# Optimization experiments

Hardware: AMD Instinct MI355X
Metric: run time of the kernel (lower is better)

The kernel has to match this reference:

```python
import jax, jax.numpy as jnp
import numpy as np

DIM = 1024
NH = 8
HD = DIM // NH  # 128
E = 8
EPS = 1e-5


def rope_cos_sin(L, hd):
    # matches RotaryPositionEmbedding: emb = cat([freqs, freqs], -1)
    inv_freq = 1.0 / (10000.0 ** (jnp.arange(0, hd, 2, dtype=jnp.float32) / hd))
    freqs = jnp.arange(L, dtype=jnp.float32)[:, None] * inv_freq[None, :]  # (L, hd/2)
    emb = jnp.concatenate([freqs, freqs], axis=-1)  # (L, hd)
    return jnp.cos(emb), jnp.sin(emb)


def rotate_half(x):
    # interleaved rotate, as in the torch apply_rope
    x1 = x[..., 0::2]
    x2 = x[..., 1::2]
    return jnp.stack((-x2, x1), axis=-1).reshape(x.shape)


def rope(t, cos, sin):
    # t: (B,H,L,D); cos/sin: (L,D)
    return t * cos[None, None] + rotate_half(t) * sin[None, None]


def heads(t):
    B, L, C = t.shape
    return t.reshape(B, L, NH, HD).transpose(0, 2, 1, 3)  # (B,H,L,D)


def setup_inputs() -> dict:
    key = jax.random.key(0)
    ks = jax.random.split(key, 32)
    std = 0.02
    d = {}
    d['x'] = jax.random.normal(ks[0], (16, 512, DIM), jnp.float32)
    d['h_a'] = jax.random.normal(ks[1], (16, 256, DIM), jnp.float32)
    d['h_t'] = jax.random.normal(ks[2], (16, 256, DIM), jnp.float32)
    names = ['qa', 'ka', 'va', 'qt', 'kt', 'vt', 'o', 'ffn']
    for i, n in enumerate(names):
        d['W_' + n] = jax.random.normal(ks[3 + 2 * i], (E, DIM, DIM), jnp.float32) * std
        d['b_' + n] = jax.random.normal(ks[4 + 2 * i], (E, DIM), jnp.float32) * std
    d['gamma'] = jnp.ones((E, DIM), jnp.float32)
    d['beta'] = jnp.zeros((E, DIM), jnp.float32)
    d['gating_factor'] = jnp.zeros((E,), jnp.float32)
    d['expert_idx'] = 3
    return d


def reference(x, h_a, h_t,
              W_qa, b_qa, W_ka, b_ka, W_va, b_va,
              W_qt, b_qt, W_kt, b_kt, W_vt, b_vt,
              W_o, b_o, W_ffn, b_ffn,
              gamma, beta, gating_factor, expert_idx):
    e = expert_idx

    def lin(t, W, b):
        return t @ W[e].T + b[e]

    B, T, C = x.shape
    Ka = h_a.shape[1]
    Kt = h_t.shape[1]

    q_a = heads(lin(x, W_qa, b_qa))        # (B,H,T,D)
    q_t = heads(lin(x, W_qt, b_qt))
    k_a = heads(lin(h_a, W_ka, b_ka))      # (B,H,Ka,D)
    v_a = heads(lin(h_a, W_va, b_va))
    k_t = heads(lin(h_t, W_kt, b_kt))      # (B,H,Kt,D)
    v_t = heads(lin(h_t, W_vt, b_vt))

    cos_m, sin_m = rope_cos_sin(T, HD)
    q_a = rope(q_a, cos_m, sin_m)
    q_t = rope(q_t, cos_m, sin_m)
    cos_a, sin_a = rope_cos_sin(Ka, HD)
    k_a = rope(k_a, cos_a, sin_a)
    cos_t, sin_t = rope_cos_sin(Kt, HD)
    k_t = rope(k_t, cos_t, sin_t)

    ratio_g = jax.nn.sigmoid(gating_factor[e])
    s_a = jnp.einsum('bhtd,bhkd->bhtk', q_a, k_a)
    s_t = jnp.einsum('bhtd,bhkd->bhtk', q_t, k_t) * ratio_g
    scores = jnp.concatenate([s_a, s_t], axis=-1) / np.sqrt(HD)
    w = jax.nn.softmax(scores, axis=-1)            # (B,H,T,Ka+Kt)
    v = jnp.concatenate([v_a, v_t], axis=2)        # (B,H,Ka+Kt,D)
    out = jnp.einsum('bhtk,bhkd->bhtd', w, v)
    out = out.transpose(0, 2, 1, 3).reshape(B, T, C)
    out = lin(out, W_o, b_o)

    x = out + x
    # ffn: SmileMoENorm -> SmileMoELinear -> ReLU (no extra residual)
    mu = jnp.mean(x, axis=-1, keepdims=True)
    var = jnp.var(x, axis=-1, keepdims=True)
    xn = (x - mu) / jnp.sqrt(var + EPS) * gamma[e] + beta[e]
    x = jax.nn.relu(lin(xn, W_ffn, b_ffn))
    return x
```

## Files before the change

kernel.cpp:

```cpp
#include <hip/hip_runtime.h>
#include <stdint.h>

typedef __bf16 bf16x8 __attribute__((ext_vector_type(8)));
typedef float f32x4 __attribute__((ext_vector_type(4)));
typedef unsigned short u16x8 __attribute__((ext_vector_type(8)));

typedef const __attribute__((address_space(1))) void* gas_ptr;
typedef __attribute__((address_space(3))) void* las_ptr;
typedef const __attribute__((address_space(3))) char* lds_c3;

__device__ __forceinline__ void gload16(const void* g, void* l) {
  __builtin_amdgcn_global_load_lds((gas_ptr)g, (las_ptr)l, 16, 0, 0);
}

__device__ __forceinline__ bf16x8 dsread16(const char* p) {
  bf16x8 r;
  asm volatile("ds_read_b128 %0, %1" : "=v"(r) : "v"((lds_c3)p));
  return r;
}
__device__ __forceinline__ void dswrite2(char* p, uint32_t v) {
  asm volatile("ds_write_b16 %0, %1" : : "v"((las_ptr)p), "v"(v));
}
template <int OFF>
__device__ __forceinline__ float dswz(float x) {
  float r;
  asm volatile("ds_swizzle_b32 %0, %1 offset:%c2" : "=v"(r) : "v"(x), "i"(OFF));
  return r;
}

__device__ __forceinline__ unsigned short f2bf(float f) {
  uint32_t u = __float_as_uint(f);
  u += 0x7FFFu + ((u >> 16) & 1u);
  return (unsigned short)(u >> 16);
}

__device__ __forceinline__ void conv8(const float* __restrict__ src,
                                      unsigned short* __restrict__ dst, int i) {
  const float4* s4 = (const float4*)src;
  float4 a = s4[2 * i], b = s4[2 * i + 1];
  u16x8 r;
  r[0] = f2bf(a.x); r[1] = f2bf(a.y); r[2] = f2bf(a.z); r[3] = f2bf(a.w);
  r[4] = f2bf(b.x); r[5] = f2bf(b.y); r[6] = f2bf(b.z); r[7] = f2bf(b.w);
  *(u16x8*)&dst[(size_t)i * 8] = r;
}

__global__ __launch_bounds__(256)
void prep_all(const float* __restrict__ x, const float* __restrict__ h_a,
              const float* __restrict__ h_t,
              const float* W0, const float* W1, const float* W2, const float* W3,
              const float* W4, const float* W5, const float* W6, const float* W7,
              const int* __restrict__ eptr,
              unsigned short* __restrict__ XB, unsigned short* __restrict__ HAB,
              unsigned short* __restrict__ HTB, unsigned short* __restrict__ WW,
              float* __restrict__ cosb, float* __restrict__ sinb) {
  const int blk = blockIdx.x, tid = threadIdx.x;
  if (blk < 4096) {
    conv8(x, XB, blk * 256 + tid);
  } else if (blk < 6144) {
    conv8(h_a, HAB, (blk - 4096) * 256 + tid);
  } else if (blk < 8192) {
    conv8(h_t, HTB, (blk - 6144) * 256 + tid);
  } else if (blk < 12288) {
    const int w = (blk - 8192) >> 9;
    const int i = ((blk - 8192) & 511) * 256 + tid;
    const float* wp;
    switch (w) {
      case 0: wp = W0; break; case 1: wp = W1; break;
      case 2: wp = W2; break; case 3: wp = W3; break;
      case 4: wp = W4; break; case 5: wp = W5; break;
      case 6: wp = W6; break; default: wp = W7; break;
    }
    conv8(wp + (size_t)(*eptr) * 1048576, WW + (size_t)w * 1048576, i);
  } else {
    const int i = (blk - 12288) * 256 + tid;
    const int t = i >> 7, d = i & 127;
    const int f = d & 63;
    float invf = expf(-0.14391156831212787f * (float)f);
    float ang = (float)t * invf;
    float s, c;
    sincosf(ang, &s, &c);
    cosb[i] = c;
    sinb[i] = s;
  }
}

template <int MODE>
__global__ __launch_bounds__(512, 1)
void gemm8p(const unsigned short* __restrict__ A0, const unsigned short* __restrict__ A1,
            const unsigned short* __restrict__ W0, const unsigned short* __restrict__ W1,
            const unsigned short* __restrict__ W2, const unsigned short* __restrict__ W3,
            const float* __restrict__ bias0, const float* __restrict__ bias1,
            const float* __restrict__ bias2, const float* __restrict__ bias3,
            const int* __restrict__ eptr, const float* __restrict__ ctab,
            const float* __restrict__ stab,
            unsigned short* __restrict__ out0, unsigned short* __restrict__ out1,
            unsigned short* __restrict__ outV) {
  __shared__ __align__(16) char AL[65536];
  __shared__ __align__(16) char BL[65536];
  const int tid = threadIdx.x;
  const int lane = tid & 63, wid = tid >> 6, fr = lane & 15, g = lane >> 4;
  const int wm = wid >> 2, wn = wid & 3;
  const int id = blockIdx.x;
  constexpr int CPX = (MODE == 0) ? 32 : 16;
  const int swz = (id & 7) * CPX + (id >> 3);
  const int bm = swz >> 3, bn = swz & 7;
  const int z = (MODE == 1) ? blockIdx.y : 0;
  const int e = *eptr;

  const unsigned short* Asel;
  const unsigned short* Wsel;
  const float* bias;
  const int half = bn >> 2;
  const int cb0 = (bn & 3) * 256;
  if constexpr (MODE == 0) {
    Asel = A0;
    Wsel = half ? W1 : W0;
    bias = (half ? bias1 : bias0) + e * 1024;
  } else {
    Asel = z ? A1 : A0;
    Wsel = z ? (half ? W3 : W2) : (half ? W1 : W0);
    bias = (z ? (half ? bias3 : bias2) : (half ? bias1 : bias0)) + e * 1024;
  }

  const char* Ab = (const char*)Asel + (size_t)bm * 256 * 2048;
  const char* Bb = (const char*)Wsel + (size_t)cb0 * 2048;

  const int csw = (((tid & 7) ^ (((tid >> 3) & 1) << 2) ^ (((tid >> 5) & 1) << 1)) << 4);
  const char* Ags = Ab + (tid >> 3) * 2048 + csw;
  const char* Bgs = Bb + (tid >> 3) * 2048 + csw;
  char* Ald = AL + tid * 16;
  char* Bld = BL + tid * 16;

#define STA(T)                                                              \
  { const char* s_ = Ags + (T) * 128;                                       \
    char* d_ = Ald + ((T) & 1) * 32768;                                     \
    gload16(s_, d_);           gload16(s_ + 131072, d_ + 8192);             \
    gload16(s_ + 262144, d_ + 16384); gload16(s_ + 393216, d_ + 24576); }
#define STB(T)                                                              \
  { const char* s_ = Bgs + (T) * 128;                                       \
    char* d_ = Bld + ((T) & 1) * 32768;                                     \
    gload16(s_, d_);           gload16(s_ + 131072, d_ + 8192);             \
    gload16(s_ + 262144, d_ + 16384); gload16(s_ + 393216, d_ + 24576); }

  const int lsw = ((fr & 1) << 2) ^ (((fr >> 2) & 1) << 1);
  const int cs0 = ((0 * 4 + g) ^ lsw) << 4;
  const int cs1 = ((1 * 4 + g) ^ lsw) << 4;
  const int arow = (wm * 128 + fr) * 128;
  const int brow = (wn * 64 + fr) * 128;

  f32x4 acc[8][4];
#pragma unroll
  for (int m = 0; m < 8; ++m)
#pragma unroll
    for (int n = 0; n < 4; ++n) acc[m][n] = f32x4{0.f, 0.f, 0.f, 0.f};
  bf16x8 af[8], bfr[2];

#define RDA(BUF, CS)                                                        \
  { const char* p_ = AL + (BUF) * 32768 + arow + (CS);                      \
    _Pragma("unroll") for (int m = 0; m < 8; ++m)                           \
        af[m] = dsread16(p_ + m * 2048); }
#define RDB(BUF, CS, NH)                                                    \
  { const char* p_ = BL + (BUF) * 32768 + brow + (NH) * 4096 + (CS);        \
    bfr[0] = dsread16(p_);                                                  \
    bfr[1] = dsread16(p_ + 2048); }

#define MF16(NH)                                                            \
  __builtin_amdgcn_s_setprio(1);                                            \
  _Pragma("unroll") for (int m = 0; m < 8; ++m) {                           \
    acc[m][(NH)*2]   = __builtin_amdgcn_mfma_f32_16x16x32_bf16(             \
        af[m], bfr[0], acc[m][(NH)*2], 0, 0, 0);                            \
    acc[m][(NH)*2+1] = __builtin_amdgcn_mfma_f32_16x16x32_bf16(             \
        af[m], bfr[1], acc[m][(NH)*2+1], 0, 0, 0);                          \
  }                                                                         \
  __builtin_amdgcn_s_setprio(0);

#define SB __builtin_amdgcn_sched_barrier(0)
#define BAR __builtin_amdgcn_s_barrier()
#define LGK0 asm volatile("s_waitcnt lgkmcnt(0)")

  STA(0); STB(0);
  SB;
  asm volatile("s_waitcnt vmcnt(0)");
  BAR;

#pragma unroll 1
  for (int t = 0; t < 16; ++t) {
    const int buf = t & 1;
    RDA(buf, cs0); RDB(buf, cs0, 0); SB;
    if (t < 15) STA(t + 1);
    SB; BAR; LGK0; SB;
    MF16(0) SB; BAR;
    RDB(buf, cs0, 1); SB;
    if (t < 15) STB(t + 1);
    SB; BAR; LGK0; SB;
    MF16(1) SB; BAR;
    RDA(buf, cs1); RDB(buf, cs1, 0); SB;
    BAR; LGK0; SB;
    MF16(0) SB; BAR;
    RDB(buf, cs1, 1); SB;
    BAR; LGK0; SB;
    MF16(1) SB;
    if (t < 15) { asm volatile("s_waitcnt vmcnt(0)"); }
    BAR;
  }
#undef RDA
#undef RDB
#undef MF16
#undef STA
#undef STB

  const int wrow0 = bm * 256 + wm * 128;
#pragma unroll
  for (int m = 0; m < 8; ++m) {
#pragma unroll
    for (int n = 0; n < 4; ++n) {
      const int gc = cb0 + wn * 64 + n * 16 + fr;
      const float bv = bias[gc];
#pragma unroll
      for (int j = 0; j < 4; ++j) {
        const int grow = wrow0 + m * 16 + g * 4 + j;
        float v = acc[m][n][j] + bv;
        if constexpr (MODE == 0) {
          const int t = grow & 511, bb = grow >> 9;
          const int hh = gc >> 7, dd = gc & 127;
          float pv = __shfl_xor(v, 1);
          float cs = ctab[t * 128 + dd], sn = stab[t * 128 + dd];
          float rh = (dd & 1) ? pv : -pv;
          float o = v * cs + rh * sn;
          unsigned short* dst = half ? out1 : out0;
          dst[(((size_t)(bb * 8 + hh) * 512 + t) << 7) + dd] = f2bf(o);
        } else {
          const int t = grow & 255, bb = grow >> 8;
          const int hh = gc >> 7, dd = gc & 127;
          if (half == 0) {
            float pv = __shfl_xor(v, 1);
            float cs = ctab[t * 128 + dd], sn = stab[t * 128 + dd];
            float rh = (dd & 1) ? pv : -pv;
            float o = v * cs + rh * sn;
            unsigned short* dst = z ? out1 : out0;
            dst[(((size_t)(bb * 8 + hh) * 256 + t) << 7) + dd] = f2bf(o);
          } else {
            outV[(((size_t)(bb * 8 + hh) << 7) + dd) * 512 + z * 256 + t] = f2bf(v);
          }
        }
      }
    }
  }
}

template <int MODE>
__global__ __launch_bounds__(512, 1)
void gemm4p(const unsigned short* __restrict__ A, const unsigned short* __restrict__ W,
            const float* __restrict__ biasb, const int* __restrict__ eptr,
            const float* __restrict__ resid, float* __restrict__ outf) {
  __shared__ __align__(16) char AL[65536];
  __shared__ __align__(16) char BL[32768];
  const int tid = threadIdx.x;
  const int lane = tid & 63, wid = tid >> 6, fr = lane & 15, g = lane >> 4;
  const int wm = wid >> 1, wn = wid & 1;
  const int id = blockIdx.x;
  const int swz = (id & 7) * 32 + (id >> 3);
  const int bm = swz >> 3, bn = swz & 7;
  const int e = *eptr;
  const float* bias = biasb + e * 1024;

  const char* Ab = (const char*)A + (size_t)bm * 256 * 2048;
  const char* Bb = (const char*)W + (size_t)bn * 128 * 2048;

  const int csw = (((tid & 7) ^ (((tid >> 3) & 1) << 2) ^ (((tid >> 5) & 1) << 1)) << 4);
  const char* Ags = Ab + (tid >> 3) * 2048 + csw;
  const char* Bgs = Bb + (tid >> 3) * 2048 + csw;
  char* Ald = AL + tid * 16;
  char* Bld = BL + tid * 16;

#define STA4(T)                                                             \
  { const char* s_ = Ags + (T) * 128;                                       \
    char* d_ = Ald + ((T) & 1) * 32768;                                     \
    gload16(s_, d_);           gload16(s_ + 131072, d_ + 8192);             \
    gload16(s_ + 262144, d_ + 16384); gload16(s_ + 393216, d_ + 24576); }
#define STB4(T)                                                             \
  { const char* s_ = Bgs + (T) * 128;                                       \
    char* d_ = Bld + ((T) & 1) * 16384;                                     \
    gload16(s_, d_);           gload16(s_ + 131072, d_ + 8192); }

  const int lsw = ((fr & 1) << 2) ^ (((fr >> 2) & 1) << 1);
  const int cs0 = ((0 * 4 + g) ^ lsw) << 4;
  const int cs1 = ((1 * 4 + g) ^ lsw) << 4;
  const int arow = (wm * 64 + fr) * 128;
  const int brow = (wn * 64 + fr) * 128;

  f32x4 acc[4][4];
#pragma unroll
  for (int m = 0; m < 4; ++m)
#pragma unroll
    for (int n = 0; n < 4; ++n) acc[m][n] = f32x4{0.f, 0.f, 0.f, 0.f};
  bf16x8 af[4], bfr[2];

#define RDA4(BUF, CS)                                                       \
  { const char* p_ = AL + (BUF) * 32768 + arow + (CS);                      \
    _Pragma("unroll") for (int m = 0; m < 4; ++m)                           \
        af[m] = dsread16(p_ + m * 2048); }
#define RDB4(BUF, CS, NH)                                                   \
  { const char* p_ = BL + (BUF) * 16384 + brow + (NH) * 4096 + (CS);        \
    bfr[0] = dsread16(p_);                                                  \
    bfr[1] = dsread16(p_ + 2048); }

#define MF8(NH)                                                             \
  __builtin_amdgcn_s_setprio(1);                                            \
  _Pragma("unroll") for (int m = 0; m < 4; ++m) {                           \
    acc[m][(NH)*2]   = __builtin_amdgcn_mfma_f32_16x16x32_bf16(             \
        af[m], bfr[0], acc[m][(NH)*2], 0, 0, 0);                            \
    acc[m][(NH)*2+1] = __builtin_amdgcn_mfma_f32_16x16x32_bf16(             \
        af[m], bfr[1], acc[m][(NH)*2+1], 0, 0, 0);                          \
  }                                                                         \
  __builtin_amdgcn_s_setprio(0);

  STA4(0); STB4(0);
  __builtin_amdgcn_sched_barrier(0);
  asm volatile("s_waitcnt vmcnt(0)");
  __builtin_amdgcn_s_barrier();

#pragma unroll 1
  for (int t = 0; t < 16; ++t) {
    const int buf = t & 1;
    RDA4(buf, cs0); RDB4(buf, cs0, 0); SB;
    if (t < 15) STA4(t + 1);
    SB; BAR; LGK0; SB;
    MF8(0) SB; BAR;
    RDB4(buf, cs0, 1); SB;
    if (t < 15) STB4(t + 1);
    SB; BAR; LGK0; SB;
    MF8(1) SB; BAR;
    RDA4(buf, cs1); RDB4(buf, cs1, 0); SB;
    BAR; LGK0; SB;
    MF8(0) SB; BAR;
    RDB4(buf, cs1, 1); SB;
    BAR; LGK0; SB;
    MF8(1) SB;
    if (t < 15) { asm volatile("s_waitcnt vmcnt(0)"); }
    BAR;
  }
#undef RDA4
#undef RDB4
#undef MF8
#undef STA4
#undef STB4
#undef SB
#undef BAR
#undef LGK0

  const int wrow0 = bm * 256 + wm * 64;
#pragma unroll
  for (int m = 0; m < 4; ++m) {
#pragma unroll
    for (int n = 0; n < 4; ++n) {
      const int gc = bn * 128 + wn * 64 + n * 16 + fr;
      const float bv = bias[gc];
#pragma unroll
      for (int j = 0; j < 4; ++j) {
        const int grow = wrow0 + m * 16 + g * 4 + j;
        float v = acc[m][n][j] + bv;
        const size_t idx = ((size_t)grow << 10) + gc;
        if constexpr (MODE == 2) outf[idx] = v + resid[idx];
        else outf[idx] = fmaxf(v, 0.f);
      }
    }
  }
}

__global__ __launch_bounds__(256, 2)
void attn_kernel(const unsigned short* __restrict__ QA, const unsigned short* __restrict__ QT,
                 const unsigned short* __restrict__ KA, const unsigned short* __restrict__ KT,
                 const unsigned short* __restrict__ VT,
                 unsigned short* __restrict__ AO,
                 const float* __restrict__ gating, const int* __restrict__ eptr) {
  __shared__ unsigned short Ks[2][8192];
  __shared__ unsigned short Vs[2][8192];
  __shared__ unsigned short Ps[8192];
  const int tid = threadIdx.x, lane = tid & 63, wv = tid >> 6;
  const int fr = lane & 15, g = lane >> 4;
  const int bid = blockIdx.x;
  const int b = bid >> 5, h = (bid >> 2) & 7, q0 = (bid & 3) << 7;
  const float ratio = 1.f / (1.f + __expf(-gating[*eptr]));
  const float SC = 0.08838834764831845f;
  const size_t bh = (size_t)(b * 8 + h);

  bf16x8 qf[2][4];
  {
    const char* qa = (const char*)QA + ((bh * 512 + q0 + wv * 32 + fr) << 8) + g * 16;
#pragma unroll
    for (int mb = 0; mb < 2; ++mb)
#pragma unroll
      for (int kb = 0; kb < 4; ++kb)
        qf[mb][kb] = *(const bf16x8*)(qa + mb * 4096 + kb * 64);
  }

  auto stage = [&](int t, int buf) {
    const char* kgb = (const char*)((t < 4) ? KA : KT) + ((bh * 256 + ((size_t)(t & 3) << 6)) << 8);
    const char* vgb = (const char*)VT + (bh << 17) + (t << 7);
    char* ksd = (char*)Ks[buf] + tid * 16;
    char* vsd = (char*)Vs[buf] + tid * 16;
#pragma unroll
    for (int j = 0; j < 4; ++j) {
      const int rk = j * 16 + (tid >> 4);
      const int ck = ((tid & 15) << 4) ^ ((rk & 7) << 4);
      gload16(kgb + rk * 256 + ck, ksd + j * 4096);
      const int dv = j * 32 + (tid >> 3);
      const int cv = ((tid & 7) << 4) ^ ((dv & 7) << 4);
      gload16(vgb + dv * 1024 + cv, vsd + j * 4096);
    }
  };

  float m_run[2][4], l_run[2][4];
  f32x4 oacc[2][8];
#pragma unroll
  for (int mb = 0; mb < 2; ++mb) {
#pragma unroll
    for (int j = 0; j < 4; ++j) { m_run[mb][j] = -1e30f; l_run[mb][j] = 0.f; }
#pragma unroll
    for (int db = 0; db < 8; ++db) oacc[mb][db] = f32x4{0.f, 0.f, 0.f, 0.f};
  }

  stage(0, 0);

  for (int it = 0; it < 8; ++it) {
    const int cur = it & 1;
    if (it < 7) stage(it + 1, cur ^ 1);
    __builtin_amdgcn_sched_barrier(0);
    if (it < 7) asm volatile("s_waitcnt vmcnt(8)");
    else        asm volatile("s_waitcnt vmcnt(0)");
    __builtin_amdgcn_sched_barrier(0);
    __builtin_amdgcn_s_barrier();
    __builtin_amdgcn_sched_barrier(0);

    if (it == 4) {
      const char* qt = (const char*)QT + ((bh * 512 + q0 + wv * 32 + fr) << 8) + g * 16;
#pragma unroll
      for (int mb = 0; mb < 2; ++mb)
#pragma unroll
        for (int kb = 0; kb < 4; ++kb)
          qf[mb][kb] = *(const bf16x8*)(qt + mb * 4096 + kb * 64);
    }
    const float sc = (it < 4) ? SC : SC * ratio;
    const char* kc = (const char*)Ks[cur];
    const char* vc = (const char*)Vs[cur];

    f32x4 s[2][4];
#pragma unroll
    for (int mb = 0; mb < 2; ++mb)
#pragma unroll
      for (int nb = 0; nb < 4; ++nb) s[mb][nb] = f32x4{0.f, 0.f, 0.f, 0.f};
    bf16x8 kfa[4], kfb[4];
#pragma unroll
    for (int kb = 0; kb < 4; ++kb) {
      const int byt = (fr * 256 + kb * 64 + g * 16) ^ ((fr & 7) << 4);
      kfa[kb] = dsread16(kc + byt);
    }
#pragma unroll
    for (int nb = 0; nb < 4; ++nb) {
      if (nb < 3) {
#pragma unroll
        for (int kb = 0; kb < 4; ++kb) {
          const int r = (nb + 1) * 16 + fr;
          const int byt = (r * 256 + kb * 64 + g * 16) ^ ((r & 7) << 4);
          if (nb & 1) kfa[kb] = dsread16(kc + byt);
          else        kfb[kb] = dsread16(kc + byt);
        }
        asm volatile("s_waitcnt lgkmcnt(4)");
      } else {
        asm volatile("s_waitcnt lgkmcnt(0)");
      }
      __builtin_amdgcn_sched_barrier(0);
      __builtin_amdgcn_s_setprio(1);
#pragma unroll
      for (int kb = 0; kb < 4; ++kb) {
        bf16x8 kf = (nb & 1) ? kfb[kb] : kfa[kb];
        s[0][nb] = __builtin_amdgcn_mfma_f32_16x16x32_bf16(qf[0][kb], kf, s[0][nb], 0, 0, 0);
        s[1][nb] = __builtin_amdgcn_mfma_f32_16x16x32_bf16(qf[1][kb], kf, s[1][nb], 0, 0, 0);
      }
      __builtin_amdgcn_s_setprio(0);
    }
    __builtin_amdgcn_sched_barrier(0);

    float red[8];
#pragma unroll
    for (int mb = 0; mb < 2; ++mb)
#pragma unroll
      for (int j = 0; j < 4; ++j) {
        float mx = -1e30f;
#pragma unroll
        for (int nb = 0; nb < 4; ++nb) {
          s[mb][nb][j] *= sc;
          mx = fmaxf(mx, s[mb][nb][j]);
        }
        red[mb * 4 + j] = mx;
      }
#define MAXR(OFF)                                                        \
    { float tmp[8];                                                      \
      _Pragma("unroll") for (int k = 0; k < 8; ++k) tmp[k] = dswz<OFF>(red[k]); \
      asm volatile("s_waitcnt lgkmcnt(0)");                              \
      __builtin_amdgcn_sched_barrier(0);                                 \
      _Pragma("unroll") for (int k = 0; k < 8; ++k) red[k] = fmaxf(red[k], tmp[k]); }
    MAXR(0x041F) MAXR(0x081F) MAXR(0x101F) MAXR(0x201F)
#undef MAXR
#pragma unroll
    for (int mb = 0; mb < 2; ++mb)
#pragma unroll
      for (int j = 0; j < 4; ++j) {
        const float mn = fmaxf(m_run[mb][j], red[mb * 4 + j]);
        const float alpha = __expf(m_run[mb][j] - mn);
        m_run[mb][j] = mn;
        l_run[mb][j] *= alpha;
#pragma unroll
        for (int db = 0; db < 8; ++db) oacc[mb][db][j] *= alpha;
      }
#pragma unroll
    for (int mb = 0; mb < 2; ++mb)
#pragma unroll
      for (int nb = 0; nb < 4; ++nb)
#pragma unroll
        for (int j = 0; j < 4; ++j) {
          float p = __expf(s[mb][nb][j] - m_run[mb][j]);
          l_run[mb][j] += p;
          const int r = wv * 32 + mb * 16 + g * 4 + j;
          const int byt = (r * 128 + (nb * 16 + fr) * 2) ^ ((r & 7) << 4);
          dswrite2((char*)Ps + byt, (uint32_t)f2bf(p));
        }

#pragma unroll
    for (int kb2 = 0; kb2 < 2; ++kb2) {
      bf16x8 pf[2], vf[8];
#pragma unroll
      for (int mb = 0; mb < 2; ++mb) {
        const int r = wv * 32 + mb * 16 + fr;
        const int byt = (r * 128 + kb2 * 64 + g * 16) ^ ((r & 7) << 4);
        pf[mb] = dsread16((const char*)Ps + byt);
      }
#pragma unroll
      for (int db = 0; db < 8; ++db) {
        const int rv = db * 16 + fr;
        const int byt = (rv * 128 + kb2 * 64 + g * 16) ^ ((rv & 7) << 4);
        vf[db] = dsread16(vc + byt);
      }
      asm volatile("s_waitcnt lgkmcnt(0)");
      __builtin_amdgcn_sched_barrier(0);
      __builtin_amdgcn_s_setprio(1);
#pragma unroll
      for (int db = 0; db < 8; ++db) {
        oacc[0][db] = __builtin_amdgcn_mfma_f32_16x16x32_bf16(pf[0], vf[db], oacc[0][db], 0, 0, 0);
        oacc[1][db] = __builtin_amdgcn_mfma_f32_16x16x32_bf16(pf[1], vf[db], oacc[1][db], 0, 0, 0);
      }
      __builtin_amdgcn_s_setprio(0);
    }
    __builtin_amdgcn_sched_barrier(0);
    __builtin_amdgcn_s_barrier();
  }

#pragma unroll
  for (int mb = 0; mb < 2; ++mb)
#pragma unroll
    for (int j = 0; j < 4; ++j) {
      float lt = l_run[mb][j];
#pragma unroll
      for (int d = 1; d < 16; d <<= 1) lt += __shfl_xor(lt, d);
      float inv = 1.f / lt;
#pragma unroll
      for (int db = 0; db < 8; ++db) {
        float o = oacc[mb][db][j] * inv;
        int row = q0 + wv * 32 + mb * 16 + g * 4 + j;
        int col = h * 128 + db * 16 + fr;
        AO[(((size_t)b * 512 + row) << 10) + col] = f2bf(o);
      }
    }
}

__global__ __launch_bounds__(256)
void ln_kernel(const float* __restrict__ X2, const float* __restrict__ gbase,
               const float* __restrict__ bbase, const int* __restrict__ eptr,
               unsigned short* __restrict__ XN) {
  const int row = blockIdx.x, tid = threadIdx.x;
  const float* x = X2 + ((size_t)row << 10);
  float4 v = ((const float4*)x)[tid];
  float s = v.x + v.y + v.z + v.w;
  float ss = v.x * v.x + v.y * v.y + v.z * v.z + v.w * v.w;
#pragma unroll
  for (int d = 1; d < 64; d <<= 1) {
    s += __shfl_xor(s, d);
    ss += __shfl_xor(ss, d);
  }
  __shared__ float red[8];
  const int wv = tid >> 6, lane = tid & 63;
  if (lane == 0) { red[wv] = s; red[4 + wv] = ss; }
  __syncthreads();
  s = red[0] + red[1] + red[2] + red[3];
  ss = red[4] + red[5] + red[6] + red[7];
  const float mu = s * 0.0009765625f;
  const float var = ss * 0.0009765625f - mu * mu;
  const float inv = rsqrtf(var + 1e-5f);
  const int e = *eptr;
  const float* gg = gbase + e * 1024 + tid * 4;
  const float* bb = bbase + e * 1024 + tid * 4;
  ushort4 o;
  o.x = f2bf((v.x - mu) * inv * gg[0] + bb[0]);
  o.y = f2bf((v.y - mu) * inv * gg[1] + bb[1]);
  o.z = f2bf((v.z - mu) * inv * gg[2] + bb[2]);
  o.w = f2bf((v.w - mu) * inv * gg[3] + bb[3]);
  *(ushort4*)&XN[((size_t)row << 10) + tid * 4] = o;
}

extern "C" void kernel_launch(void* const* d_in, const int* in_sizes, int n_in,
                              void* d_out, int out_size, void* d_ws, size_t ws_size,
                              hipStream_t stream) {
  (void)in_sizes; (void)n_in; (void)out_size; (void)ws_size;
  const float* x      = (const float*)d_in[0];
  const float* h_a    = (const float*)d_in[1];
  const float* h_t    = (const float*)d_in[2];
  const float* W_qa   = (const float*)d_in[3];
  const float* b_qa   = (const float*)d_in[4];
  const float* W_ka   = (const float*)d_in[5];
  const float* b_ka   = (const float*)d_in[6];
  const float* W_va   = (const float*)d_in[7];
  const float* b_va   = (const float*)d_in[8];
  const float* W_qt   = (const float*)d_in[9];
  const float* b_qt   = (const float*)d_in[10];
  const float* W_kt   = (const float*)d_in[11];
  const float* b_kt   = (const float*)d_in[12];
  const float* W_vt   = (const float*)d_in[13];
  const float* b_vt   = (const float*)d_in[14];
  const float* W_o    = (const float*)d_in[15];
  const float* b_o    = (const float*)d_in[16];
  const float* W_ffn  = (const float*)d_in[17];
  const float* b_ffn  = (const float*)d_in[18];
  const float* gamma  = (const float*)d_in[19];
  const float* beta   = (const float*)d_in[20];
  const float* gating = (const float*)d_in[21];
  const int*   eptr   = (const int*)d_in[22];

  char* ws = (char*)d_ws;
  unsigned short* XB  = (unsigned short*)(ws + 0);
  unsigned short* HAB = (unsigned short*)(ws + 16777216);
  unsigned short* HTB = (unsigned short*)(ws + 25165824);
  float*          X2  = (float*)(ws + 0);
  unsigned short* WW  = (unsigned short*)(ws + 33554432);
  unsigned short* QAb = (unsigned short*)(ws + 50331648);
  unsigned short* XN  = QAb;
  unsigned short* QTb = (unsigned short*)(ws + 67108864);
  unsigned short* KAb = (unsigned short*)(ws + 83886080);
  unsigned short* KTb = (unsigned short*)(ws + 92274688);
  unsigned short* VTb = (unsigned short*)(ws + 100663296);
  unsigned short* AOb = (unsigned short*)(ws + 117440512);
  float* COS = (float*)(ws + 134217728);
  float* SIN = (float*)(ws + 134479872);

  prep_all<<<12544, 256, 0, stream>>>(x, h_a, h_t,
      W_qa, W_ka, W_va, W_qt, W_kt, W_vt, W_o, W_ffn, eptr,
      XB, HAB, HTB, WW, COS, SIN);

  gemm8p<0><<<dim3(256), 512, 0, stream>>>(XB, nullptr,
      WW + 0ull * 1048576, WW + 3ull * 1048576, nullptr, nullptr,
      b_qa, b_qt, nullptr, nullptr, eptr, COS, SIN,
      QAb, QTb, nullptr);

  gemm8p<1><<<dim3(128, 2), 512, 0, stream>>>(HAB, HTB,
      WW + 1ull * 1048576, WW + 2ull * 1048576,
      WW + 4ull * 1048576, WW + 5ull * 1048576,
      b_ka, b_va, b_kt, b_vt, eptr, COS, SIN,
      KAb, KTb, VTb);

  attn_kernel<<<512, 256, 0, stream>>>(QAb, QTb, KAb, KTb, VTb, AOb, gating, eptr);

  gemm4p<2><<<dim3(256), 512, 0, stream>>>(AOb, WW + 6ull * 1048576, b_o, eptr, x, X2);

  ln_kernel<<<8192, 256, 0, stream>>>(X2, gamma, beta, eptr, XN);

  gemm4p<3><<<dim3(256), 512, 0, stream>>>(XN, WW + 7ull * 1048576, b_ffn, eptr,
                                           nullptr, (float*)d_out);
}
```

Before: 237.0 us.

## Unify GEMMs into triple-buffered 256x128 kernel with fewer barriers

Replaces the two GEMM kernels with a single templated kernel that uses 256x128 tiles, a three-stage LDS ring (prefetch two k-steps ahead with a partial vmcnt wait), and one barrier per k-step instead of several. The LDS swizzle becomes a full 3-bit XOR, and the k-halves are split between wave groups. The projection GEMMs now launch twice as many smaller blocks. The aim is to hide global-load latency and cut synchronisation stalls, at the cost of lower per-block reuse in the QKV GEMMs and more LDS.

```diff
diff --git a/kernel.cpp b/kernel.cpp
--- a/kernel.cpp
+++ b/kernel.cpp
@@ -33,6 +33,10 @@
   u += 0x7FFFu + ((u >> 16) & 1u);
   return (unsigned short)(u >> 16);
 }
+
+#define SB __builtin_amdgcn_sched_barrier(0)
+#define BAR __builtin_amdgcn_s_barrier()
+#define LGK0 asm volatile("s_waitcnt lgkmcnt(0)")
 
 __device__ __forceinline__ void conv8(const float* __restrict__ src,
                                       unsigned short* __restrict__ dst, int i) {
@@ -86,7 +90,7 @@
 
 template <int MODE>
 __global__ __launch_bounds__(512, 1)
-void gemm8p(const unsigned short* __restrict__ A0, const unsigned short* __restrict__ A1,
+void gemm3r(const unsigned short* __restrict__ A0, const unsigned short* __restrict__ A1,
             const unsigned short* __restrict__ W0, const unsigned short* __restrict__ W1,
             const unsigned short* __restrict__ W2, const unsigned short* __restrict__ W3,
             const float* __restrict__ bias0, const float* __restrict__ bias1,
@@ -94,127 +98,128 @@
             const int* __restrict__ eptr, const float* __restrict__ ctab,
             const float* __restrict__ stab,
             unsigned short* __restrict__ out0, unsigned short* __restrict__ out1,
-            unsigned short* __restrict__ outV) {
-  __shared__ __align__(16) char AL[65536];
-  __shared__ __align__(16) char BL[65536];
+            unsigned short* __restrict__ outV,
+            const float* __restrict__ resid, float* __restrict__ outf) {
+  __shared__ __align__(16) char AL[98304];
+  __shared__ __align__(16) char BL[49152];
   const int tid = threadIdx.x;
   const int lane = tid & 63, wid = tid >> 6, fr = lane & 15, g = lane >> 4;
-  const int wm = wid >> 2, wn = wid & 3;
+  const int wm = wid >> 1, wn = wid & 1;
   const int id = blockIdx.x;
-  constexpr int CPX = (MODE == 0) ? 32 : 16;
+  constexpr int CPX = (MODE == 0) ? 64 : 32;
   const int swz = (id & 7) * CPX + (id >> 3);
-  const int bm = swz >> 3, bn = swz & 7;
+  constexpr int NBNS = (MODE <= 1) ? 4 : 3;
+  const int bm = swz >> NBNS;
+  const int bn = swz & ((1 << NBNS) - 1);
   const int z = (MODE == 1) ? blockIdx.y : 0;
   const int e = *eptr;
 
   const unsigned short* Asel;
   const unsigned short* Wsel;
   const float* bias;
-  const int half = bn >> 2;
-  const int cb0 = (bn & 3) * 256;
+  int half = 0, cb0;
   if constexpr (MODE == 0) {
     Asel = A0;
+    half = bn >> 3;
     Wsel = half ? W1 : W0;
     bias = (half ? bias1 : bias0) + e * 1024;
-  } else {
+    cb0 = (bn & 7) * 128;
+  } else if constexpr (MODE == 1) {
     Asel = z ? A1 : A0;
+    half = bn >> 3;
     Wsel = z ? (half ? W3 : W2) : (half ? W1 : W0);
     bias = (z ? (half ? bias3 : bias2) : (half ? bias1 : bias0)) + e * 1024;
+    cb0 = (bn & 7) * 128;
+  } else {
+    Asel = A0;
+    Wsel = W0;
+    bias = bias0 + e * 1024;
+    cb0 = bn * 128;
   }
 
   const char* Ab = (const char*)Asel + (size_t)bm * 256 * 2048;
   const char* Bb = (const char*)Wsel + (size_t)cb0 * 2048;
 
-  const int csw = (((tid & 7) ^ (((tid >> 3) & 1) << 2) ^ (((tid >> 5) & 1) << 1)) << 4);
+  const int csw = (((tid & 7) ^ ((tid >> 3) & 7)) << 4);
   const char* Ags = Ab + (tid >> 3) * 2048 + csw;
   const char* Bgs = Bb + (tid >> 3) * 2048 + csw;
   char* Ald = AL + tid * 16;
   char* Bld = BL + tid * 16;
 
-#define STA(T)                                                              \
+#define STA(T, BUF)                                                         \
   { const char* s_ = Ags + (T) * 128;                                       \
-    char* d_ = Ald + ((T) & 1) * 32768;                                     \
-    gload16(s_, d_);           gload16(s_ + 131072, d_ + 8192);             \
+    char* d_ = Ald + (BUF) * 32768;                                         \
+    gload16(s_, d_);                  gload16(s_ + 131072, d_ + 8192);      \
     gload16(s_ + 262144, d_ + 16384); gload16(s_ + 393216, d_ + 24576); }
-#define STB(T)                                                              \
+#define STB(T, BUF)                                                         \
   { const char* s_ = Bgs + (T) * 128;                                       \
-    char* d_ = Bld + ((T) & 1) * 32768;                                     \
-    gload16(s_, d_);           gload16(s_ + 131072, d_ + 8192);             \
-    gload16(s_ + 262144, d_ + 16384); gload16(s_ + 393216, d_ + 24576); }
-
-  const int lsw = ((fr & 1) << 2) ^ (((fr >> 2) & 1) << 1);
-  const int cs0 = ((0 * 4 + g) ^ lsw) << 4;
-  const int cs1 = ((1 * 4 + g) ^ lsw) << 4;
-  const int arow = (wm * 128 + fr) * 128;
+    char* d_ = Bld + (BUF) * 16384;                                         \
+    gload16(s_, d_);                  gload16(s_ + 131072, d_ + 8192); }
+
+  const int lsw7 = fr & 7;
+  const int ksel = (wid & 4) ? 4 : 0;
+  const int cA = ((ksel + g) ^ lsw7) << 4;
+  const int cB = (((4 - ksel) + g) ^ lsw7) << 4;
+  const int arow = (wm * 64 + fr) * 128;
   const int brow = (wn * 64 + fr) * 128;
 
-  f32x4 acc[8][4];
-#pragma unroll
-  for (int m = 0; m < 8; ++m)
+  f32x4 acc[4][4];
+#pragma unroll
+  for (int m = 0; m < 4; ++m)
 #pragma unroll
     for (int n = 0; n < 4; ++n) acc[m][n] = f32x4{0.f, 0.f, 0.f, 0.f};
-  bf16x8 af[8], bfr[2];
-
-#define RDA(BUF, CS)                                                        \
-  { const char* p_ = AL + (BUF) * 32768 + arow + (CS);                      \
-    _Pragma("unroll") for (int m = 0; m < 8; ++m)                           \
-        af[m] = dsread16(p_ + m * 2048); }
-#define RDB(BUF, CS, NH)                                                    \
-  { const char* p_ = BL + (BUF) * 32768 + brow + (NH) * 4096 + (CS);        \
-    bfr[0] = dsread16(p_);                                                  \
-    bfr[1] = dsread16(p_ + 2048); }
-
-#define MF16(NH)                                                            \
+  bf16x8 af[4], bf[4];
+
+#define RDAB(BASEA, BASEB, C)                                               \
+  { const char* pa_ = (BASEA) + arow + (C);                                 \
+    const char* pb_ = (BASEB) + brow + (C);                                 \
+    _Pragma("unroll") for (int m = 0; m < 4; ++m)                           \
+        af[m] = dsread16(pa_ + m * 2048);                                   \
+    _Pragma("unroll") for (int n = 0; n < 4; ++n)                           \
+        bf[n] = dsread16(pb_ + n * 2048); }
+
+#define MF16                                                                \
   __builtin_amdgcn_s_setprio(1);                                            \
-  _Pragma("unroll") for (int m = 0; m < 8; ++m) {                           \
-    acc[m][(NH)*2]   = __builtin_amdgcn_mfma_f32_16x16x32_bf16(             \
-        af[m], bfr[0], acc[m][(NH)*2], 0, 0, 0);                            \
-    acc[m][(NH)*2+1] = __builtin_amdgcn_mfma_f32_16x16x32_bf16(             \
-        af[m], bfr[1], acc[m][(NH)*2+1], 0, 0, 0);                          \
-  }                                                                         \
+  _Pragma("unroll") for (int m = 0; m < 4; ++m)                             \
+    _Pragma("unroll") for (int n = 0; n < 4; ++n)                           \
+        acc[m][n] = __builtin_amdgcn_mfma_f32_16x16x32_bf16(                \
+            af[m], bf[n], acc[m][n], 0, 0, 0);                              \
   __builtin_amdgcn_s_setprio(0);
 
-#define SB __builtin_amdgcn_sched_barrier(0)
-#define BAR __builtin_amdgcn_s_barrier()
-#define LGK0 asm volatile("s_waitcnt lgkmcnt(0)")
-
-  STA(0); STB(0);
-  SB;
-  asm volatile("s_waitcnt vmcnt(0)");
-  BAR;
-
+  STA(0, 0); STB(0, 0); STA(1, 1); STB(1, 1);
+
+  int bc = 0;
 #pragma unroll 1
   for (int t = 0; t < 16; ++t) {
-    const int buf = t & 1;
-    RDA(buf, cs0); RDB(buf, cs0, 0); SB;
-    if (t < 15) STA(t + 1);
-    SB; BAR; LGK0; SB;
-    MF16(0) SB; BAR;
-    RDB(buf, cs0, 1); SB;
-    if (t < 15) STB(t + 1);
-    SB; BAR; LGK0; SB;
-    MF16(1) SB; BAR;
-    RDA(buf, cs1); RDB(buf, cs1, 0); SB;
-    BAR; LGK0; SB;
-    MF16(0) SB; BAR;
-    RDB(buf, cs1, 1); SB;
-    BAR; LGK0; SB;
-    MF16(1) SB;
-    if (t < 15) { asm volatile("s_waitcnt vmcnt(0)"); }
-    BAR;
-  }
-#undef RDA
-#undef RDB
+    SB;
+    if (t <= 14) asm volatile("s_waitcnt vmcnt(6)");
+    else         asm volatile("s_waitcnt vmcnt(0)");
+    BAR; SB;
+    const char* ALc = AL + bc * 32768;
+    const char* BLc = BL + bc * 16384;
+    const int bs = bc ? bc - 1 : 2;
+    RDAB(ALc, BLc, cA); SB;
+    if (t <= 13) STA(t + 2, bs);
+    SB; LGK0; SB;
+    MF16 SB;
+    RDAB(ALc, BLc, cB); SB;
+    if (t <= 13) STB(t + 2, bs);
+    SB; LGK0; SB;
+    MF16 SB;
+    bc = (bc == 2) ? 0 : bc + 1;
+  }
+#undef RDAB
 #undef MF16
 #undef STA
 #undef STB
 
-  const int wrow0 = bm * 256 + wm * 128;
-#pragma unroll
-  for (int m = 0; m < 8; ++m) {
+  const int wrow0 = bm * 256 + wm * 64;
+#pragma unroll
+  for (int m = 0; m < 4; ++m) {
 #pragma unroll
     for (int n = 0; n < 4; ++n) {
-      const int gc = cb0 + wn * 64 + n * 16 + fr;
+      const int lc = wn * 64 + n * 16 + fr;
+      const int gc = cb0 + lc;
       const float bv = bias[gc];
 #pragma unroll
       for (int j = 0; j < 4; ++j) {
@@ -229,7 +234,7 @@
           float o = v * cs + rh * sn;
           unsigned short* dst = half ? out1 : out0;
           dst[(((size_t)(bb * 8 + hh) * 512 + t) << 7) + dd] = f2bf(o);
-        } else {
+        } else if constexpr (MODE == 1) {
           const int t = grow & 255, bb = grow >> 8;
           const int hh = gc >> 7, dd = gc & 127;
           if (half == 0) {
@@ -242,127 +247,11 @@
           } else {
             outV[(((size_t)(bb * 8 + hh) << 7) + dd) * 512 + z * 256 + t] = f2bf(v);
           }
+        } else {
+          const size_t idx = ((size_t)grow << 10) + gc;
+          if constexpr (MODE == 2) outf[idx] = v + resid[idx];
+          else outf[idx] = fmaxf(v, 0.f);
         }
-      }
-    }
-  }
-}
-
-template <int MODE>
-__global__ __launch_bounds__(512, 1)
-void gemm4p(const unsigned short* __restrict__ A, const unsigned short* __restrict__ W,
-            const float* __restrict__ biasb, const int* __restrict__ eptr,
-            const float* __restrict__ resid, float* __restrict__ outf) {
-  __shared__ __align__(16) char AL[65536];
-  __shared__ __align__(16) char BL[32768];
-  const int tid = threadIdx.x;
-  const int lane = tid & 63, wid = tid >> 6, fr = lane & 15, g = lane >> 4;
-  const int wm = wid >> 1, wn = wid & 1;
-  const int id = blockIdx.x;
-  const int swz = (id & 7) * 32 + (id >> 3);
-  const int bm = swz >> 3, bn = swz & 7;
-  const int e = *eptr;
-  const float* bias = biasb + e * 1024;
-
-  const char* Ab = (const char*)A + (size_t)bm * 256 * 2048;
-  const char* Bb = (const char*)W + (size_t)bn * 128 * 2048;
-
-  const int csw = (((tid & 7) ^ (((tid >> 3) & 1) << 2) ^ (((tid >> 5) & 1) << 1)) << 4);
-  const char* Ags = Ab + (tid >> 3) * 2048 + csw;
-  const char* Bgs = Bb + (tid >> 3) * 2048 + csw;
-  char* Ald = AL + tid * 16;
-  char* Bld = BL + tid * 16;
-
-#define STA4(T)                                                             \
-  { const char* s_ = Ags + (T) * 128;                                       \
-    char* d_ = Ald + ((T) & 1) * 32768;                                     \
-    gload16(s_, d_);           gload16(s_ + 131072, d_ + 8192);             \
-    gload16(s_ + 262144, d_ + 16384); gload16(s_ + 393216, d_ + 24576); }
-#define STB4(T)                                                             \
-  { const char* s_ = Bgs + (T) * 128;                                       \
-    char* d_ = Bld + ((T) & 1) * 16384;                                     \
-    gload16(s_, d_);           gload16(s_ + 131072, d_ + 8192); }
-
-  const int lsw = ((fr & 1) << 2) ^ (((fr >> 2) & 1) << 1);
-  const int cs0 = ((0 * 4 + g) ^ lsw) << 4;
-  const int cs1 = ((1 * 4 + g) ^ lsw) << 4;
-  const int arow = (wm * 64 + fr) * 128;
-  const int brow = (wn * 64 + fr) * 128;
-
-  f32x4 acc[4][4];
-#pragma unroll
-  for (int m = 0; m < 4; ++m)
-#pragma unroll
-    for (int n = 0; n < 4; ++n) acc[m][n] = f32x4{0.f, 0.f, 0.f, 0.f};
-  bf16x8 af[4], bfr[2];
-
-#define RDA4(BUF, CS)                                                       \
-  { const char* p_ = AL + (BUF) * 32768 + arow + (CS);                      \
-    _Pragma("unroll") for (int m = 0; m < 4; ++m)                           \
-        af[m] = dsread16(p_ + m * 2048); }
-#define RDB4(BUF, CS, NH)                                                   \
-  { const char* p_ = BL + (BUF) * 16384 + brow + (NH) * 4096 + (CS);        \
-    bfr[0] = dsread16(p_);                                                  \
-    bfr[1] = dsread16(p_ + 2048); }
-
-#define MF8(NH)                                                             \
-  __builtin_amdgcn_s_setprio(1);                                            \
-  _Pragma("unroll") for (int m = 0; m < 4; ++m) {                           \
-    acc[m][(NH)*2]   = __builtin_amdgcn_mfma_f32_16x16x32_bf16(             \
-        af[m], bfr[0], acc[m][(NH)*2], 0, 0, 0);                            \
-    acc[m][(NH)*2+1] = __builtin_amdgcn_mfma_f32_16x16x32_bf16(             \
-        af[m], bfr[1], acc[m][(NH)*2+1], 0, 0, 0);                          \
-  }                                                                         \
-  __builtin_amdgcn_s_setprio(0);
-
-  STA4(0); STB4(0);
-  __builtin_amdgcn_sched_barrier(0);
-  asm volatile("s_waitcnt vmcnt(0)");
-  __builtin_amdgcn_s_barrier();
-
-#pragma unroll 1
-  for (int t = 0; t < 16; ++t) {
-    const int buf = t & 1;
-    RDA4(buf, cs0); RDB4(buf, cs0, 0); SB;
-    if (t < 15) STA4(t + 1);
-    SB; BAR; LGK0; SB;
-    MF8(0) SB; BAR;
-    RDB4(buf, cs0, 1); SB;
-    if (t < 15) STB4(t + 1);
-    SB; BAR; LGK0; SB;
-    MF8(1) SB; BAR;
-    RDA4(buf, cs1); RDB4(buf, cs1, 0); SB;
-    BAR; LGK0; SB;
-    MF8(0) SB; BAR;
-    RDB4(buf, cs1, 1); SB;
-    BAR; LGK0; SB;
-    MF8(1) SB;
-    if (t < 15) { asm volatile("s_waitcnt vmcnt(0)"); }
-    BAR;
-  }
-#undef RDA4
-#undef RDB4
-#undef MF8
-#undef STA4
-#undef STB4
-#undef SB
-#undef BAR
-#undef LGK0
-
-  const int wrow0 = bm * 256 + wm * 64;
-#pragma unroll
-  for (int m = 0; m < 4; ++m) {
-#pragma unroll
-    for (int n = 0; n < 4; ++n) {
-      const int gc = bn * 128 + wn * 64 + n * 16 + fr;
-      const float bv = bias[gc];
-#pragma unroll
-      for (int j = 0; j < 4; ++j) {
-        const int grow = wrow0 + m * 16 + g * 4 + j;
-        float v = acc[m][n][j] + bv;
-        const size_t idx = ((size_t)grow << 10) + gc;
-        if constexpr (MODE == 2) outf[idx] = v + resid[idx];
-        else outf[idx] = fmaxf(v, 0.f);
       }
     }
   }
@@ -426,12 +315,12 @@
   for (int it = 0; it < 8; ++it) {
     const int cur = it & 1;
     if (it < 7) stage(it + 1, cur ^ 1);
-    __builtin_amdgcn_sched_barrier(0);
+    SB;
     if (it < 7) asm volatile("s_waitcnt vmcnt(8)");
     else        asm volatile("s_waitcnt vmcnt(0)");
-    __builtin_amdgcn_sched_barrier(0);
-    __builtin_amdgcn_s_barrier();
-    __builtin_amdgcn_sched_barrier(0);
+    SB;
+    BAR;
+    SB;
 
     if (it == 4) {
       const char* qt = (const char*)QT + ((bh * 512 + q0 + wv * 32 + fr) << 8) + g * 16;
@@ -470,7 +359,7 @@
       } else {
         asm volatile("s_waitcnt lgkmcnt(0)");
       }
-      __builtin_amdgcn_sched_barrier(0);
+      SB;
       __builtin_amdgcn_s_setprio(1);
 #pragma unroll
       for (int kb = 0; kb < 4; ++kb) {
@@ -480,7 +369,7 @@
       }
       __builtin_amdgcn_s_setprio(0);
     }
-    __builtin_amdgcn_sched_barrier(0);
+    SB;
 
     float red[8];
 #pragma unroll
@@ -499,7 +388,7 @@
     { float tmp[8];                                                      \
       _Pragma("unroll") for (int k = 0; k < 8; ++k) tmp[k] = dswz<OFF>(red[k]); \
       asm volatile("s_waitcnt lgkmcnt(0)");                              \
-      __builtin_amdgcn_sched_barrier(0);                                 \
+      SB;                                                                \
       _Pragma("unroll") for (int k = 0; k < 8; ++k) red[k] = fmaxf(red[k], tmp[k]); }
     MAXR(0x041F) MAXR(0x081F) MAXR(0x101F) MAXR(0x201F)
 #undef MAXR
@@ -543,7 +432,7 @@
         vf[db] = dsread16(vc + byt);
       }
       asm volatile("s_waitcnt lgkmcnt(0)");
-      __builtin_amdgcn_sched_barrier(0);
+      SB;
       __builtin_amdgcn_s_setprio(1);
 #pragma unroll
       for (int db = 0; db < 8; ++db) {
@@ -552,8 +441,8 @@
       }
       __builtin_amdgcn_s_setprio(0);
     }
-    __builtin_amdgcn_sched_barrier(0);
-    __builtin_amdgcn_s_barrier();
+    SB;
+    BAR;
   }
 
 #pragma unroll
@@ -656,23 +545,28 @@
       W_qa, W_ka, W_va, W_qt, W_kt, W_vt, W_o, W_ffn, eptr,
       XB, HAB, HTB, WW, COS, SIN);
 
-  gemm8p<0><<<dim3(256), 512, 0, stream>>>(XB, nullptr,
+  gemm3r<0><<<dim3(512), 512, 0, stream>>>(XB, nullptr,
       WW + 0ull * 1048576, WW + 3ull * 1048576, nullptr, nullptr,
       b_qa, b_qt, nullptr, nullptr, eptr, COS, SIN,
-      QAb, QTb, nullptr);
-
-  gemm8p<1><<<dim3(128, 2), 512, 0, stream>>>(HAB, HTB,
+      QAb, QTb, nullptr, nullptr, nullptr);
+
+  gemm3r<1><<<dim3(256, 2), 512, 0, stream>>>(HAB, HTB,
       WW + 1ull * 1048576, WW + 2ull * 1048576,
       WW + 4ull * 1048576, WW + 5ull * 1048576,
       b_ka, b_va, b_kt, b_vt, eptr, COS, SIN,
-      KAb, KTb, VTb);
+      KAb, KTb, VTb, nullptr, nullptr);
 
   attn_kernel<<<512, 256, 0, stream>>>(QAb, QTb, KAb, KTb, VTb, AOb, gating, eptr);
 
-  gemm4p<2><<<dim3(256), 512, 0, stream>>>(AOb, WW + 6ull * 1048576, b_o, eptr, x, X2);
+  gemm3r<2><<<dim3(256), 512, 0, stream>>>(AOb, nullptr,
+      WW + 6ull * 1048576, nullptr, nullptr, nullptr,
+      b_o, nullptr, nullptr, nullptr, eptr, nullptr, nullptr,
+      nullptr, nullptr, nullptr, x, X2);
 
   ln_kernel<<<8192, 256, 0, stream>>>(X2, gamma, beta, eptr, XN);
 
-  gemm4p<3><<<dim3(256), 512, 0, stream>>>(XN, WW + 7ull * 1048576, b_ffn, eptr,
-                                           nullptr, (float*)d_out);
-}
+  gemm3r<3><<<dim3(256), 512, 0, stream>>>(XN, nullptr,
+      WW + 7ull * 1048576, nullptr, nullptr, nullptr,
+      b_ffn, nullptr, nullptr, nullptr, eptr, nullptr, nullptr,
+      nullptr, nullptr, nullptr, nullptr, (float*)d_out);
+}
```

Measured after the change: 223.6 us. -5.6%, faster.
